# Performance work log

Hardware: AMD Instinct MI355X
Metric: run time of the kernel (lower is better)

Reference implementation:

```python
import jax, jax.numpy as jnp
import numpy as np

B, S, D = 4, 2048, 1024
H = 16
HD = D // H  # 64


def setup_inputs() -> dict:
    key = jax.random.key(0)
    k0, k1, k2, k3, k4 = jax.random.split(key, 5)
    scale = 1.0 / np.sqrt(D)
    return {
        "x": jax.random.normal(k0, (B, S, D), dtype=jnp.float32),
        "Wq": jax.random.normal(k1, (D, D), dtype=jnp.float32) * scale,
        "Wk": jax.random.normal(k2, (D, D), dtype=jnp.float32) * scale,
        "Wv": jax.random.normal(k3, (D, D), dtype=jnp.float32) * scale,
        "Wo": jax.random.normal(k4, (D, D), dtype=jnp.float32) * scale,
    }


def reference(x, Wq, Wk, Wv, Wo):
    # nn.Linear(bias=False): y = x @ W.T, W is [out, in]
    def proj(W):
        y = jnp.einsum('bsd,ed->bse', x, W)          # [B,S,D]
        return y.reshape(B, S, H, HD).transpose(0, 2, 1, 3)  # [B,H,S,HD]

    q, k, v = proj(Wq), proj(Wk), proj(Wv)
    scores = jnp.einsum('bhqd,bhkd->bhqk', q, k) / np.sqrt(HD)  # [B,H,S,S]
    attn = jax.nn.softmax(scores, axis=-1)
    out = jnp.einsum('bhqk,bhkd->bhqd', attn, v)     # [B,H,S,HD]
    out = out.transpose(0, 2, 1, 3).reshape(B, S, D)  # [B,S,D]
    return jnp.einsum('bsd,ed->bse', out, Wo)
```

## Files before the change

### kernel.cpp

```cpp
#include <hip/hip_runtime.h>
#include <hip/hip_bf16.h>
#include <cstdint>
#include <cstddef>

#define DEV __device__ __forceinline__

typedef __attribute__((ext_vector_type(8))) __bf16 bfrag8;
typedef __attribute__((ext_vector_type(4))) float f32x4;
typedef __attribute__((ext_vector_type(8))) unsigned short u16x8;
typedef __attribute__((ext_vector_type(4))) unsigned short u16x4;

static constexpr int S = 2048, D = 1024;
static constexpr size_t XN = (size_t)4 * 2048 * 1024;
static constexpr size_t WN = (size_t)1024 * 1024;

DEV unsigned short bfu(float f) {
  return __builtin_bit_cast(unsigned short, (__bf16)f);
}

#define GLOAD16(g, l)                                                          \
  __builtin_amdgcn_global_load_lds(                                            \
      (const __attribute__((address_space(1))) void*)(g),                      \
      (__attribute__((address_space(3))) void*)(l), 16, 0, 0)

#define VMW4 asm volatile("s_waitcnt vmcnt(4)" ::: "memory")
#define VMW0 asm volatile("s_waitcnt vmcnt(0)" ::: "memory")
#define BAR()                                                                  \
  do {                                                                         \
    asm volatile("" ::: "memory");                                             \
    __builtin_amdgcn_s_barrier();                                              \
    asm volatile("" ::: "memory");                                             \
  } while (0)

__global__ __launch_bounds__(256) void convert_kernel(
    const float* __restrict__ x, const float* __restrict__ wq,
    const float* __restrict__ wk, const float* __restrict__ wv,
    const float* __restrict__ wo, unsigned short* __restrict__ dst) {
  size_t i = ((size_t)blockIdx.x * 256 + threadIdx.x) * 8;
  const float* src;
  size_t off;
  if (i < XN) { src = x; off = i; }
  else if (i < XN + WN)     { src = wq; off = i - XN; }
  else if (i < XN + 2 * WN) { src = wk; off = i - (XN + WN); }
  else if (i < XN + 3 * WN) { src = wv; off = i - (XN + 2 * WN); }
  else                      { src = wo; off = i - (XN + 3 * WN); }
  const float4* p = (const float4*)(src + off);
  float4 a = p[0], b = p[1];
  u16x8 o;
  o[0] = bfu(a.x); o[1] = bfu(a.y); o[2] = bfu(a.z); o[3] = bfu(a.w);
  o[4] = bfu(b.x); o[5] = bfu(b.y); o[6] = bfu(b.z); o[7] = bfu(b.w);
  *(u16x8*)(dst + i) = o;
}

DEV void gemm_mainloop(const unsigned short* __restrict__ Ag,
                       const unsigned short* __restrict__ Bg,
                       unsigned short* ldsA, unsigned short* ldsB,
                       f32x4 (&acc)[4][4], int tid) {
  const int lane = tid & 63;
  const int wr = (tid >> 7) & 1;
  const int wc = (tid >> 6) & 1;
  for (int kt = 0; kt < 32; ++kt) {
#pragma unroll
    for (int i = 0; i < 2; ++i) {
      const int c = tid + i * 256;
      const int row = c >> 2, ks = c & 3;
      const int ldsoff = ((tid & ~63) + i * 256) * 16;
      GLOAD16(Ag + (size_t)row * 1024 + kt * 32 + ks * 8, (char*)ldsA + ldsoff);
      GLOAD16(Bg + (size_t)row * 1024 + kt * 32 + ks * 8, (char*)ldsB + ldsoff);
    }
    asm volatile("s_waitcnt vmcnt(0)" ::: "memory");
    __syncthreads();
    bfrag8 av[4], bv[4];
#pragma unroll
    for (int m = 0; m < 4; ++m)
      av[m] = *(const bfrag8*)(ldsA + (wr * 64 + m * 16 + (lane & 15)) * 32 +
                               (lane >> 4) * 8);
#pragma unroll
    for (int n = 0; n < 4; ++n)
      bv[n] = *(const bfrag8*)(ldsB + (wc * 64 + n * 16 + (lane & 15)) * 32 +
                               (lane >> 4) * 8);
#pragma unroll
    for (int m = 0; m < 4; ++m)
#pragma unroll
      for (int n = 0; n < 4; ++n)
        acc[m][n] =
            __builtin_amdgcn_mfma_f32_16x16x32_bf16(av[m], bv[n], acc[m][n], 0, 0, 0);
    __syncthreads();
  }
}

__global__ __launch_bounds__(256, 2) void gemm_qkv(
    const unsigned short* __restrict__ xbf, const unsigned short* __restrict__ wq,
    const unsigned short* __restrict__ wk, const unsigned short* __restrict__ wv,
    unsigned short* __restrict__ Qb, unsigned short* __restrict__ Kb,
    unsigned short* __restrict__ Vt) {
  __shared__ __align__(16) unsigned short ldsA[128 * 32];
  __shared__ __align__(16) unsigned short ldsB[128 * 32];
  const int tid = threadIdx.x;
  const int z = blockIdx.z;
  const unsigned short* W = (z == 0) ? wq : ((z == 1) ? wk : wv);
  const int m0 = blockIdx.y * 128, n0 = blockIdx.x * 128;

  f32x4 acc[4][4];
#pragma unroll
  for (int m = 0; m < 4; ++m)
#pragma unroll
    for (int n = 0; n < 4; ++n) acc[m][n] = (f32x4){0.f, 0.f, 0.f, 0.f};

  gemm_mainloop(xbf + (size_t)m0 * 1024, W + (size_t)n0 * 1024, ldsA, ldsB, acc, tid);

  const int lane = tid & 63;
  const int wr = (tid >> 7) & 1, wc = (tid >> 6) & 1;
  const int hi = lane >> 4, lo = lane & 15;
  if (z < 2) {
    unsigned short* dst = (z == 0) ? Qb : Kb;
#pragma unroll
    for (int m = 0; m < 4; ++m)
#pragma unroll
      for (int n = 0; n < 4; ++n)
#pragma unroll
        for (int r = 0; r < 4; ++r) {
          int row = m0 + wr * 64 + m * 16 + hi * 4 + r;
          int col = n0 + wc * 64 + n * 16 + lo;
          dst[(size_t)row * 1024 + col] = bfu(acc[m][n][r]);
        }
  } else {
#pragma unroll
    for (int m = 0; m < 4; ++m)
#pragma unroll
      for (int n = 0; n < 4; ++n) {
        int col = n0 + wc * 64 + n * 16 + lo;
        int hh = col >> 6, hd = col & 63;
        int row0 = m0 + wr * 64 + m * 16 + hi * 4;
        int b_ = row0 >> 11, s_ = row0 & 2047;
        u16x4 pk;
#pragma unroll
        for (int r = 0; r < 4; ++r) pk[r] = bfu(acc[m][n][r]);
        *(u16x4*)(Vt + ((size_t)((b_ * 16 + hh) * 64 + hd)) * 2048 + s_) = pk;
      }
  }
}

__global__ __launch_bounds__(256, 2) void gemm_out(
    const unsigned short* __restrict__ Ob, const unsigned short* __restrict__ wo,
    float* __restrict__ out) {
  __shared__ __align__(16) unsigned short ldsA[128 * 32];
  __shared__ __align__(16) unsigned short ldsB[128 * 32];
  const int tid = threadIdx.x;
  const int m0 = blockIdx.y * 128, n0 = blockIdx.x * 128;
  f32x4 acc[4][4];
#pragma unroll
  for (int m = 0; m < 4; ++m)
#pragma unroll
    for (int n = 0; n < 4; ++n) acc[m][n] = (f32x4){0.f, 0.f, 0.f, 0.f};
  gemm_mainloop(Ob + (size_t)m0 * 1024, wo + (size_t)n0 * 1024, ldsA, ldsB, acc, tid);
  const int lane = tid & 63;
  const int wr = (tid >> 7) & 1, wc = (tid >> 6) & 1;
  const int hi = lane >> 4, lo = lane & 15;
#pragma unroll
  for (int m = 0; m < 4; ++m)
#pragma unroll
    for (int n = 0; n < 4; ++n)
#pragma unroll
      for (int r = 0; r < 4; ++r) {
        int row = m0 + wr * 64 + m * 16 + hi * 4 + r;
        int col = n0 + wc * 64 + n * 16 + lo;
        out[(size_t)row * 1024 + col] = acc[m][n][r];
      }
}

__global__ __launch_bounds__(256, 2) void attn_kernel(
    const unsigned short* __restrict__ Qb, const unsigned short* __restrict__ Kb,
    const unsigned short* __restrict__ Vt, unsigned short* __restrict__ Ob) {
  __shared__ __align__(16) unsigned short Plds[4 * 16 * 64];
  __shared__ __align__(16) unsigned short K0[64 * 64];
  __shared__ __align__(16) unsigned short K1[64 * 64];
  __shared__ __align__(16) unsigned short V0[64 * 64];
  __shared__ __align__(16) unsigned short V1[64 * 64];

  const int tid = threadIdx.x, lane = tid & 63, wave = tid >> 6;
  const int hi = lane >> 4, lo = lane & 15;

  const int lin = blockIdx.x;
  const int wid = (lin & 7) * 128 + (lin >> 3);
  const int bh = wid >> 4, qt = wid & 15;
  const int b = bh >> 4, h = bh & 15;

  const unsigned short* Qg = Qb + (size_t)(b * S + qt * 128) * D + h * 64;
  const unsigned short* Kg = Kb + (size_t)b * S * D + h * 64;
  const unsigned short* Vg = Vt + (size_t)bh * 64 * S;
  unsigned short* Pw = Plds + wave * 16 * 64;

  bfrag8 qf[2][2];
#pragma unroll
  for (int m = 0; m < 2; ++m)
#pragma unroll
    for (int kk = 0; kk < 2; ++kk)
      qf[m][kk] =
          *(const bfrag8*)(Qg + (size_t)(wave * 32 + m * 16 + lo) * D + kk * 32 + hi * 8);

  f32x4 oA[2][4];
  float mrow[2][4], lrow[2][4];
#pragma unroll
  for (int m = 0; m < 2; ++m) {
#pragma unroll
    for (int n = 0; n < 4; ++n) oA[m][n] = (f32x4){0.f, 0.f, 0.f, 0.f};
#pragma unroll
    for (int r = 0; r < 4; ++r) { mrow[m][r] = -INFINITY; lrow[m][r] = 0.f; }
  }
  const float c1 = 0.125f * 1.4426950408889634f;

  auto stage = [&](unsigned short* kl, unsigned short* vl, int kv0) {
#pragma unroll
    for (int i = 0; i < 2; ++i) {
      int c = tid + i * 256;
      int row = c >> 3, sl = (c & 7) ^ (row & 7);
      int ldsoff = ((tid & ~63) + i * 256) * 16;
      GLOAD16(Kg + (size_t)(kv0 + row) * D + sl * 8, (char*)kl + ldsoff);
      GLOAD16(Vg + (size_t)row * S + kv0 + sl * 8, (char*)vl + ldsoff);
    }
  };

  auto compute = [&](const unsigned short* Kc, const unsigned short* Vc) {
    bfrag8 kf[4][2];
#pragma unroll
    for (int n = 0; n < 4; ++n)
#pragma unroll
      for (int kk = 0; kk < 2; ++kk) {
        int row = n * 16 + lo;
        int slot = (kk * 4 + hi) ^ (row & 7);
        kf[n][kk] = *(const bfrag8*)(Kc + row * 64 + slot * 8);
      }
    f32x4 sc[2][4];
#pragma unroll
    for (int m = 0; m < 2; ++m)
#pragma unroll
      for (int n = 0; n < 4; ++n) {
        sc[m][n] = (f32x4){0.f, 0.f, 0.f, 0.f};
#pragma unroll
        for (int kk = 0; kk < 2; ++kk)
          sc[m][n] = __builtin_amdgcn_mfma_f32_16x16x32_bf16(qf[m][kk], kf[n][kk],
                                                             sc[m][n], 0, 0, 0);
      }

#pragma unroll
    for (int m = 0; m < 2; ++m)
#pragma unroll
      for (int r = 0; r < 4; ++r) {
        float mx = fmaxf(fmaxf(sc[m][0][r], sc[m][1][r]),
                         fmaxf(sc[m][2][r], sc[m][3][r]));
        mx = fmaxf(mx, __shfl_xor(mx, 1));
        mx = fmaxf(mx, __shfl_xor(mx, 2));
        mx = fmaxf(mx, __shfl_xor(mx, 4));
        mx = fmaxf(mx, __shfl_xor(mx, 8));
        float Mnew = fmaxf(mrow[m][r], mx * c1);
        float alpha = __builtin_amdgcn_exp2f(mrow[m][r] - Mnew);
        float psum = 0.f;
#pragma unroll
        for (int n = 0; n < 4; ++n) {
          float p = __builtin_amdgcn_exp2f(sc[m][n][r] * c1 - Mnew);
          sc[m][n][r] = p;
          psum += p;
        }
        psum += __shfl_xor(psum, 1);
        psum += __shfl_xor(psum, 2);
        psum += __shfl_xor(psum, 4);
        psum += __shfl_xor(psum, 8);
        lrow[m][r] = lrow[m][r] * alpha + psum;
        mrow[m][r] = Mnew;
#pragma unroll
        for (int n = 0; n < 4; ++n) oA[m][n][r] *= alpha;
      }

    bfrag8 vf[4][2];
#pragma unroll
    for (int n = 0; n < 4; ++n)
#pragma unroll
      for (int kk = 0; kk < 2; ++kk) {
        int row = n * 16 + lo;
        int slot = (kk * 4 + hi) ^ (row & 7);
        vf[n][kk] = *(const bfrag8*)(Vc + row * 64 + slot * 8);
      }

#pragma unroll
    for (int m = 0; m < 2; ++m) {
#pragma unroll
      for (int n = 0; n < 4; ++n)
#pragma unroll
        for (int r = 0; r < 4; ++r) {
          int q = hi * 4 + r;
          int kv = n * 16 + lo;
          int sl = (kv >> 3) ^ (q & 7);
          Pw[q * 64 + sl * 8 + (kv & 7)] = bfu(sc[m][n][r]);
        }
      bfrag8 pf[2];
#pragma unroll
      for (int kk = 0; kk < 2; ++kk) {
        int slot = (kk * 4 + hi) ^ (lo & 7);
        pf[kk] = *(const bfrag8*)(Pw + lo * 64 + slot * 8);
      }
#pragma unroll
      for (int n = 0; n < 4; ++n)
#pragma unroll
        for (int kk = 0; kk < 2; ++kk)
          oA[m][n] = __builtin_amdgcn_mfma_f32_16x16x32_bf16(pf[kk], vf[n][kk],
                                                             oA[m][n], 0, 0, 0);
    }
  };

  stage(K0, V0, 0);
  for (int t = 0; t < 32; t += 2) {
    stage(K1, V1, (t + 1) * 64);
    VMW4;
    BAR();
    compute(K0, V0);
    BAR();
    if (t + 2 < 32) {
      stage(K0, V0, (t + 2) * 64);
      VMW4;
    } else {
      VMW0;
    }
    BAR();
    compute(K1, V1);
    BAR();
  }

#pragma unroll
  for (int m = 0; m < 2; ++m)
#pragma unroll
    for (int r = 0; r < 4; ++r) {
      float inv = 1.f / lrow[m][r];
      int q = wave * 32 + m * 16 + hi * 4 + r;
      size_t rowbase = (size_t)(b * S + qt * 128 + q) * D + h * 64;
#pragma unroll
      for (int n = 0; n < 4; ++n)
        Ob[rowbase + n * 16 + lo] = bfu(oA[m][n][r] * inv);
    }
}

extern "C" void kernel_launch(void* const* d_in, const int* in_sizes, int n_in,
                              void* d_out, int out_size, void* d_ws, size_t ws_size,
                              hipStream_t stream) {
  const float* x = (const float*)d_in[0];
  const float* wq = (const float*)d_in[1];
  const float* wk = (const float*)d_in[2];
  const float* wv = (const float*)d_in[3];
  const float* wo = (const float*)d_in[4];
  float* out = (float*)d_out;

  unsigned short* base = (unsigned short*)d_ws;
  unsigned short* xbf = base;
  unsigned short* wqb = xbf + XN;
  unsigned short* wkb = wqb + WN;
  unsigned short* wvb = wkb + WN;
  unsigned short* wob = wvb + WN;
  unsigned short* Qb = wob + WN;
  unsigned short* Kb = Qb + XN;
  unsigned short* Vt = Kb + XN;
  unsigned short* Ob = Vt + XN;

  convert_kernel<<<dim3(6144), dim3(256), 0, stream>>>(x, wq, wk, wv, wo, xbf);
  gemm_qkv<<<dim3(8, 64, 3), dim3(256), 0, stream>>>(xbf, wqb, wkb, wvb, Qb, Kb, Vt);
  attn_kernel<<<dim3(1024), dim3(256), 0, stream>>>(Qb, Kb, Vt, Ob);
  gemm_out<<<dim3(8, 64), dim3(256), 0, stream>>>(Ob, wob, out);
}
```

Baseline: 392.0 us.

## Compute transposed S^T and O^T in attention to keep P in registers

Swaps MFMA operand order so scores come out transposed (kv rows, query columns), which makes each query's softmax stats a per-lane scalar. The max and sum reductions shrink to two cross-lane shuffles, and the P matrix is repacked into the bf16 B-operand through register shuffles instead of a round trip through LDS. Output is accumulated as O^T and written with 8-byte vector stores. This removes the LDS P buffer and its bank traffic but adds shuffle and select instructions per tile.

```diff
diff --git a/kernel.cpp b/kernel.cpp
--- a/kernel.cpp
+++ b/kernel.cpp
@@ -9,6 +9,7 @@
 typedef __attribute__((ext_vector_type(4))) float f32x4;
 typedef __attribute__((ext_vector_type(8))) unsigned short u16x8;
 typedef __attribute__((ext_vector_type(4))) unsigned short u16x4;
+typedef __attribute__((ext_vector_type(4))) unsigned int u32x4;
 
 static constexpr int S = 2048, D = 1024;
 static constexpr size_t XN = (size_t)4 * 2048 * 1024;
@@ -172,7 +173,6 @@
 __global__ __launch_bounds__(256, 2) void attn_kernel(
     const unsigned short* __restrict__ Qb, const unsigned short* __restrict__ Kb,
     const unsigned short* __restrict__ Vt, unsigned short* __restrict__ Ob) {
-  __shared__ __align__(16) unsigned short Plds[4 * 16 * 64];
   __shared__ __align__(16) unsigned short K0[64 * 64];
   __shared__ __align__(16) unsigned short K1[64 * 64];
   __shared__ __align__(16) unsigned short V0[64 * 64];
@@ -189,7 +189,6 @@
   const unsigned short* Qg = Qb + (size_t)(b * S + qt * 128) * D + h * 64;
   const unsigned short* Kg = Kb + (size_t)b * S * D + h * 64;
   const unsigned short* Vg = Vt + (size_t)bh * 64 * S;
-  unsigned short* Pw = Plds + wave * 16 * 64;
 
   bfrag8 qf[2][2];
 #pragma unroll
@@ -199,16 +198,14 @@
       qf[m][kk] =
           *(const bfrag8*)(Qg + (size_t)(wave * 32 + m * 16 + lo) * D + kk * 32 + hi * 8);
 
-  f32x4 oA[2][4];
-  float mrow[2][4], lrow[2][4];
-#pragma unroll
-  for (int m = 0; m < 2; ++m) {
-#pragma unroll
-    for (int n = 0; n < 4; ++n) oA[m][n] = (f32x4){0.f, 0.f, 0.f, 0.f};
-#pragma unroll
-    for (int r = 0; r < 4; ++r) { mrow[m][r] = -INFINITY; lrow[m][r] = 0.f; }
-  }
-  const float c1 = 0.125f * 1.4426950408889634f;
+  f32x4 oT[4][2];
+  float mrow[2], lrow[2];
+#pragma unroll
+  for (int n = 0; n < 4; ++n)
+#pragma unroll
+    for (int m = 0; m < 2; ++m) oT[n][m] = (f32x4){0.f, 0.f, 0.f, 0.f};
+  mrow[0] = mrow[1] = -__builtin_inff();
+  lrow[0] = lrow[1] = 0.f;
 
   auto stage = [&](unsigned short* kl, unsigned short* vl, int kv0) {
 #pragma unroll
@@ -222,89 +219,89 @@
   };
 
   auto compute = [&](const unsigned short* Kc, const unsigned short* Vc) {
+    const float c1 = 0.125f * 1.4426950408889634f;
     bfrag8 kf[4][2];
 #pragma unroll
     for (int n = 0; n < 4; ++n)
 #pragma unroll
       for (int kk = 0; kk < 2; ++kk) {
         int row = n * 16 + lo;
-        int slot = (kk * 4 + hi) ^ (row & 7);
-        kf[n][kk] = *(const bfrag8*)(Kc + row * 64 + slot * 8);
-      }
-    f32x4 sc[2][4];
-#pragma unroll
-    for (int m = 0; m < 2; ++m)
-#pragma unroll
-      for (int n = 0; n < 4; ++n) {
-        sc[m][n] = (f32x4){0.f, 0.f, 0.f, 0.f};
+        kf[n][kk] = *(const bfrag8*)(Kc + row * 64 + (((kk * 4 + hi) ^ (row & 7)) * 8));
+      }
+    f32x4 sc[4][2];
+#pragma unroll
+    for (int n = 0; n < 4; ++n)
+#pragma unroll
+      for (int m = 0; m < 2; ++m) {
+        sc[n][m] = (f32x4){0.f, 0.f, 0.f, 0.f};
 #pragma unroll
         for (int kk = 0; kk < 2; ++kk)
-          sc[m][n] = __builtin_amdgcn_mfma_f32_16x16x32_bf16(qf[m][kk], kf[n][kk],
-                                                             sc[m][n], 0, 0, 0);
-      }
-
-#pragma unroll
-    for (int m = 0; m < 2; ++m)
-#pragma unroll
-      for (int r = 0; r < 4; ++r) {
-        float mx = fmaxf(fmaxf(sc[m][0][r], sc[m][1][r]),
-                         fmaxf(sc[m][2][r], sc[m][3][r]));
-        mx = fmaxf(mx, __shfl_xor(mx, 1));
-        mx = fmaxf(mx, __shfl_xor(mx, 2));
-        mx = fmaxf(mx, __shfl_xor(mx, 4));
-        mx = fmaxf(mx, __shfl_xor(mx, 8));
-        float Mnew = fmaxf(mrow[m][r], mx * c1);
-        float alpha = __builtin_amdgcn_exp2f(mrow[m][r] - Mnew);
-        float psum = 0.f;
-#pragma unroll
-        for (int n = 0; n < 4; ++n) {
-          float p = __builtin_amdgcn_exp2f(sc[m][n][r] * c1 - Mnew);
-          sc[m][n][r] = p;
-          psum += p;
-        }
-        psum += __shfl_xor(psum, 1);
-        psum += __shfl_xor(psum, 2);
-        psum += __shfl_xor(psum, 4);
-        psum += __shfl_xor(psum, 8);
-        lrow[m][r] = lrow[m][r] * alpha + psum;
-        mrow[m][r] = Mnew;
-#pragma unroll
-        for (int n = 0; n < 4; ++n) oA[m][n][r] *= alpha;
-      }
-
+          sc[n][m] = __builtin_amdgcn_mfma_f32_16x16x32_bf16(kf[n][kk], qf[m][kk],
+                                                             sc[n][m], 0, 0, 0);
+      }
     bfrag8 vf[4][2];
 #pragma unroll
     for (int n = 0; n < 4; ++n)
 #pragma unroll
       for (int kk = 0; kk < 2; ++kk) {
         int row = n * 16 + lo;
-        int slot = (kk * 4 + hi) ^ (row & 7);
-        vf[n][kk] = *(const bfrag8*)(Vc + row * 64 + slot * 8);
+        vf[n][kk] = *(const bfrag8*)(Vc + row * 64 + (((kk * 4 + hi) ^ (row & 7)) * 8));
       }
 
 #pragma unroll
     for (int m = 0; m < 2; ++m) {
+      float mx = sc[0][m][0];
+#pragma unroll
+      for (int n = 0; n < 4; ++n)
+#pragma unroll
+        for (int r = 0; r < 4; ++r)
+          if (!(n == 0 && r == 0)) mx = fmaxf(mx, sc[n][m][r]);
+      mx = fmaxf(mx, __shfl_xor(mx, 16));
+      mx = fmaxf(mx, __shfl_xor(mx, 32));
+      float Mnew = fmaxf(mrow[m], mx * c1);
+      float alpha = __builtin_amdgcn_exp2f(mrow[m] - Mnew);
+      float ps = 0.f;
 #pragma unroll
       for (int n = 0; n < 4; ++n)
 #pragma unroll
         for (int r = 0; r < 4; ++r) {
-          int q = hi * 4 + r;
-          int kv = n * 16 + lo;
-          int sl = (kv >> 3) ^ (q & 7);
-          Pw[q * 64 + sl * 8 + (kv & 7)] = bfu(sc[m][n][r]);
+          float p = __builtin_amdgcn_exp2f(sc[n][m][r] * c1 - Mnew);
+          sc[n][m][r] = p;
+          ps += p;
         }
-      bfrag8 pf[2];
+      ps += __shfl_xor(ps, 16);
+      ps += __shfl_xor(ps, 32);
+      lrow[m] = lrow[m] * alpha + ps;
+      mrow[m] = Mnew;
+#pragma unroll
+      for (int n = 0; n < 4; ++n)
+#pragma unroll
+        for (int r = 0; r < 4; ++r) oT[n][m][r] *= alpha;
+
+      unsigned int pku[4][2];
+#pragma unroll
+      for (int n = 0; n < 4; ++n)
+#pragma unroll
+        for (int rp = 0; rp < 2; ++rp)
+          pku[n][rp] = (unsigned int)bfu(sc[n][m][2 * rp]) |
+                       ((unsigned int)bfu(sc[n][m][2 * rp + 1]) << 16);
+
 #pragma unroll
       for (int kk = 0; kk < 2; ++kk) {
-        int slot = (kk * 4 + hi) ^ (lo & 7);
-        pf[kk] = *(const bfrag8*)(Pw + lo * 64 + slot * 8);
-      }
-#pragma unroll
-      for (int n = 0; n < 4; ++n)
-#pragma unroll
-        for (int kk = 0; kk < 2; ++kk)
-          oA[m][n] = __builtin_amdgcn_mfma_f32_16x16x32_bf16(pf[kk], vf[n][kk],
-                                                             oA[m][n], 0, 0, 0);
+        u32x4 pw;
+#pragma unroll
+        for (int dw = 0; dw < 4; ++dw) {
+          int src = ((2 * (hi & 1) + (dw >> 1)) << 4) | lo;
+          unsigned int v0 = (unsigned int)__shfl((int)pku[2 * kk][dw & 1], src);
+          unsigned int v1 = (unsigned int)__shfl((int)pku[2 * kk + 1][dw & 1], src);
+          pw[dw] = (hi >> 1) ? v1 : v0;
+        }
+        bfrag8 pb = __builtin_bit_cast(bfrag8, pw);
+#pragma unroll
+        for (int n = 0; n < 4; ++n)
+          oT[n][m] = __builtin_amdgcn_mfma_f32_16x16x32_bf16(vf[n][kk], pb,
+                                                             oT[n][m], 0, 0, 0);
+      }
     }
   };
 
@@ -327,16 +324,17 @@
   }
 
 #pragma unroll
-  for (int m = 0; m < 2; ++m)
-#pragma unroll
-    for (int r = 0; r < 4; ++r) {
-      float inv = 1.f / lrow[m][r];
-      int q = wave * 32 + m * 16 + hi * 4 + r;
-      size_t rowbase = (size_t)(b * S + qt * 128 + q) * D + h * 64;
-#pragma unroll
-      for (int n = 0; n < 4; ++n)
-        Ob[rowbase + n * 16 + lo] = bfu(oA[m][n][r] * inv);
-    }
+  for (int m = 0; m < 2; ++m) {
+    float inv = 1.f / lrow[m];
+    size_t qrow = (size_t)(b * S + qt * 128 + wave * 32 + m * 16 + lo) * D + h * 64;
+#pragma unroll
+    for (int n = 0; n < 4; ++n) {
+      u16x4 p4;
+#pragma unroll
+      for (int r = 0; r < 4; ++r) p4[r] = bfu(oT[n][m][r] * inv);
+      *(u16x4*)(Ob + qrow + n * 16 + hi * 4) = p4;
+    }
+  }
 }
 
 extern "C" void kernel_launch(void* const* d_in, const int* in_sizes, int n_in,
```

Result: faster. 324.8 us (-17.1%).
